# Kernel tuning notes

Measured on AMD Instinct MI355X. Metric: run time of the kernel, lower is better.

The kernel has to match this reference:

```python
import jax, jax.numpy as jnp
import numpy as np

S, N, F_IN, F_OUT = 8, 4096, 128, 128


def setup_inputs() -> dict:
    key = jax.random.key(0)
    ks = jax.random.split(key, 7)
    return {
        "theta": jax.random.normal(ks[0], (S,), dtype=jnp.float32),
        "T_slices": jax.random.normal(ks[1], (S, N, N), dtype=jnp.float32),
        "x": jax.random.normal(ks[2], (N, F_IN), dtype=jnp.float32),
        "a": jax.random.uniform(ks[3], (N, N), dtype=jnp.float32),
        "W_fc": jax.random.normal(ks[4], (F_OUT, F_IN), dtype=jnp.float32) * (1.0 / np.sqrt(F_IN)),
        "b_fc": jax.random.normal(ks[5], (F_OUT,), dtype=jnp.float32) * 0.01,
        "prelu_alpha": jnp.full((F_IN,), 0.25, dtype=jnp.float32),
    }


def reference(theta, T_slices, x, a, W_fc, b_fc, prelu_alpha):
    # q = sum_s theta[s] * T_slices[s]  -> [N, N]
    q = jnp.einsum("s,snm->nm", theta, T_slices)
    # mask by adjacency (the torch code then converts to sparse; math is identical)
    q = q * a
    # diffused features: [N, N] @ [N, F_in] -> [N, F_in]
    out = q @ x
    # per-channel PReLU over the feature dim (num_parameters = input_dim)
    out = jnp.where(out >= 0, out, prelu_alpha * out)
    # final linear: out @ W_fc.T + b_fc -> [N, F_out]
    return out @ W_fc.T + b_fc
```

## Files before the change

### kernel.cpp

```cpp
#include <hip/hip_runtime.h>
#include <stdint.h>

constexpr int N  = 4096;
constexpr int F  = 128;
constexpr int S  = 8;
constexpr int BM = 16;
constexpr int KSPLIT = 8;
constexpr int KRANGE = N / KSPLIT;
constexpr int BK = 32;
constexpr int NCH = KRANGE / BK;
constexpr int NT = 256;

typedef float f4  __attribute__((ext_vector_type(4)));
typedef float f2  __attribute__((ext_vector_type(2)));
typedef short bf16x8 __attribute__((ext_vector_type(8)));
typedef unsigned short us4 __attribute__((ext_vector_type(4)));

__device__ __forceinline__ unsigned short f2bf(float f) {
  union { float f; unsigned int u; } v; v.f = f;
  unsigned int u = v.u + 0x7FFFu + ((v.u >> 16) & 1u);
  return (unsigned short)(u >> 16);
}

__device__ __forceinline__ void bar_sync() {
  asm volatile("s_waitcnt lgkmcnt(0)" ::: "memory");
  __builtin_amdgcn_s_barrier();
  asm volatile("" ::: "memory");
}

__device__ __forceinline__ void vm_drain() {
  asm volatile("s_waitcnt vmcnt(0)" ::: "memory");
}

__device__ __forceinline__ void vm_wait7() {
  asm volatile("s_waitcnt vmcnt(7)" ::: "memory");
}

__device__ __forceinline__ void gload_lds16(const void* g, void* l) {
  __builtin_amdgcn_global_load_lds(
      (const __attribute__((address_space(1))) void*)g,
      (__attribute__((address_space(3))) void*)l, 16, 0, 0);
}

__global__ __launch_bounds__(256, 2) void ggd_xt(
    const float* __restrict__ x, unsigned short* __restrict__ xT) {
  __shared__ float xl[64][132];
  const int t  = threadIdx.x;
  const int k0 = blockIdx.x * 64;

  {
    const int kr = t >> 2, fs = (t & 3) * 32;
    const float* src = x + (size_t)(k0 + kr) * F + fs;
#pragma unroll
    for (int i = 0; i < 8; ++i)
      *(f4*)&xl[kr][fs + i * 4] = *(const f4*)(src + i * 4);
  }
  __syncthreads();
  {
    const int f = t >> 1, kh = (t & 1) * 32;
    us4 o[8];
#pragma unroll
    for (int i = 0; i < 32; ++i)
      o[i >> 2][i & 3] = f2bf(xl[kh + i][f]);
    unsigned short* dst = xT + (size_t)f * N + k0 + kh;
#pragma unroll
    for (int j = 0; j < 8; ++j)
      *(us4*)(dst + j * 4) = o[j];
  }
}

template <bool USE_WS>
__global__ __launch_bounds__(NT, 2) void ggd_diffuse(
    const float* __restrict__ theta,
    const float* __restrict__ Ts,
    const unsigned short* __restrict__ xT,
    const float* __restrict__ a,
    float* __restrict__ dst)
{
  __shared__ float rawT[2][S][BM][BK];
  __shared__ unsigned short xt_lds[3][F][BK];
  __shared__ unsigned short q_lds[2][BM][BK];

  const int t  = threadIdx.x;
  const int rb = blockIdx.x >> 3;
  const int ks = blockIdx.x & 7;
  const int n0 = rb * BM;
  const int k0 = ks * KRANGE;

  float th[S];
#pragma unroll
  for (int s = 0; s < S; ++s) th[s] = theta[s];

  const int wave = t >> 6, lane = t & 63;
  const size_t slice = (size_t)N * N;

  const int qr = t >> 4;
  const int qk = (t & 15) * 2;

  f4 acc[2];
#pragma unroll
  for (int i = 0; i < 2; ++i) acc[i] = (f4)(0.f);

  auto stage_rawT = [&](int c, int buf) {
    const size_t cb = (size_t)(k0 + c * BK) + (lane & 7) * 4;
    const int grow = lane >> 3;
#pragma unroll
    for (int j = 0; j < 4; ++j) {
      const int i = wave * 4 + j;
      const int s = i >> 1;
      const int row = (i & 1) * 8 + grow;
      const float* src = Ts + (size_t)s * slice + (size_t)(n0 + row) * N + cb;
      gload_lds16(src, &rawT[buf][0][0][0] + i * 256);
    }
  };

  auto stage_x = [&](int c, int buf) {
    const uint8_t* xb = (const uint8_t*)xT;
    const size_t kbyte = (size_t)(k0 + c * BK) * 2;
#pragma unroll
    for (int j = 0; j < 2; ++j) {
      const int i = wave * 2 + j;
      const int fr = i * 16 + (lane >> 2);
      const uint8_t* src = xb + (size_t)fr * (N * 2) + kbyte + (lane & 3) * 16;
      gload_lds16(src, &xt_lds[buf][i * 16][0]);
    }
  };

  auto load_a = [&](int c) -> f2 {
    return *(const f2*)(a + (size_t)(n0 + qr) * N + (k0 + c * BK + qk));
  };

  auto qgen = [&](int c1, f2 av) {
    const float* rt = &rawT[c1 & 1][0][qr][qk];
    f2 sum;
    {
      f2 tv = *(const f2*)(rt);
      sum[0] = th[0] * tv[0];
      sum[1] = th[0] * tv[1];
    }
#pragma unroll
    for (int s = 1; s < S; ++s) {
      f2 tv = *(const f2*)(rt + (size_t)s * (BM * BK));
      sum[0] = fmaf(th[s], tv[0], sum[0]);
      sum[1] = fmaf(th[s], tv[1], sum[1]);
    }
    const unsigned int packed =
        (unsigned int)f2bf(av[0] * sum[0]) |
        ((unsigned int)f2bf(av[1] * sum[1]) << 16);
    *(unsigned int*)&q_lds[c1 & 1][qr][qk] = packed;
  };

  auto compute = [&](int c) {
    const unsigned short* qb = &q_lds[c & 1][0][0];
    bf16x8 af = *(const bf16x8*)(qb + (lane & 15) * BK + (lane >> 4) * 8);
    const unsigned short* xb = &xt_lds[c % 3][0][0];
#pragma unroll
    for (int i = 0; i < 2; ++i) {
      const int ft = wave * 2 + i;
      bf16x8 bf = *(const bf16x8*)(xb + (size_t)(ft * 16 + (lane & 15)) * BK +
                                   (lane >> 4) * 8);
      acc[i] = __builtin_amdgcn_mfma_f32_16x16x32_bf16(af, bf, acc[i], 0, 0, 0);
    }
  };

  f2 avE, avO;
  stage_rawT(0, 0);
  stage_x(0, 0);
  avE = load_a(0);
  stage_rawT(1, 1);
  stage_x(1, 1);
  avO = load_a(1);
  vm_drain();
  bar_sync();
  qgen(0, avE);
  bar_sync();

  auto body = [&](int c, f2& av_iss, f2 av_use) {
    const bool iss = (c + 2 < NCH);
    if (iss) {
      stage_rawT(c + 2, c & 1);
      stage_x(c + 2, (c + 2) % 3);
      av_iss = load_a(c + 2);
    }
    compute(c);
    if (iss) vm_wait7(); else vm_drain();
    bar_sync();
    if (c + 1 < NCH) qgen(c + 1, av_use);
    bar_sync();
  };

  for (int cc = 0; cc < NCH; cc += 2) {
    body(cc,     avE, avO);
    body(cc + 1, avO, avE);
  }

  const int crow = n0 + (lane >> 4) * 4;
  const int ccol = lane & 15;
#pragma unroll
  for (int i = 0; i < 2; ++i) {
    const int fo = (wave * 2 + i) * 16 + ccol;
#pragma unroll
    for (int r = 0; r < 4; ++r) {
      const size_t row = (size_t)(crow + r);
      if (USE_WS) {
        dst[((size_t)ks * N + row) * F + fo] = acc[i][r];
      } else {
        atomicAdd(dst + row * F + fo, acc[i][r]);
      }
    }
  }
}

template <bool USE_WS>
__global__ __launch_bounds__(256, 2) void ggd_fc(
    const float* __restrict__ W,
    const float* __restrict__ bfc,
    const float* __restrict__ alpha,
    const float* __restrict__ src,
    float* __restrict__ out)
{
  __shared__ float p_lds[16 * F];
  const int t  = threadIdx.x;
  const int n0 = blockIdx.x * 16;

  {
    const int lr = t >> 4, c8 = (t & 15) * 8;
    f4 v0, v1;
    if (USE_WS) {
      v0 = (f4)(0.f); v1 = (f4)(0.f);
#pragma unroll
      for (int ks = 0; ks < KSPLIT; ++ks) {
        const float* sp = src + ((size_t)ks * N + n0 + lr) * F + c8;
        v0 += *(const f4*)(sp);
        v1 += *(const f4*)(sp + 4);
      }
    } else {
      const float* ip = src + (size_t)(n0 + lr) * F + c8;
      v0 = *(const f4*)(ip);
      v1 = *(const f4*)(ip + 4);
    }
    f4 a0 = *(const f4*)(alpha + c8);
    f4 a1 = *(const f4*)(alpha + c8 + 4);
#pragma unroll
    for (int j = 0; j < 4; ++j) {
      v0[j] = v0[j] >= 0.f ? v0[j] : a0[j] * v0[j];
      v1[j] = v1[j] >= 0.f ? v1[j] : a1[j] * v1[j];
    }
    *(f4*)&p_lds[lr * F + c8]     = v0;
    *(f4*)&p_lds[lr * F + c8 + 4] = v1;
  }
  __syncthreads();

  const int r2  = t >> 5;
  const int fo0 = (t & 31) * 4;
  f4 accA = *(const f4*)(bfc + fo0);
  f4 accB = accA;
#pragma unroll 4
  for (int fi4 = 0; fi4 < F / 4; ++fi4) {
    f4 pA = *(const f4*)&p_lds[r2 * F + fi4 * 4];
    f4 pB = *(const f4*)&p_lds[(r2 + 8) * F + fi4 * 4];
#pragma unroll
    for (int e = 0; e < 4; ++e) {
      f4 wv = *(const f4*)(W + (size_t)(fo0 + e) * F + fi4 * 4);
      accA[e] = fmaf(pA[0], wv[0], fmaf(pA[1], wv[1],
                fmaf(pA[2], wv[2], fmaf(pA[3], wv[3], accA[e]))));
      accB[e] = fmaf(pB[0], wv[0], fmaf(pB[1], wv[1],
                fmaf(pB[2], wv[2], fmaf(pB[3], wv[3], accB[e]))));
    }
  }
  *(f4*)(out + (size_t)(n0 + r2) * F + fo0)     = accA;
  *(f4*)(out + (size_t)(n0 + r2 + 8) * F + fo0) = accB;
}

extern "C" void kernel_launch(void* const* d_in, const int* in_sizes, int n_in,
                              void* d_out, int out_size, void* d_ws, size_t ws_size,
                              hipStream_t stream) {
  const float* theta = (const float*)d_in[0];
  const float* Ts    = (const float*)d_in[1];
  const float* x     = (const float*)d_in[2];
  const float* a     = (const float*)d_in[3];
  const float* W     = (const float*)d_in[4];
  const float* bfc   = (const float*)d_in[5];
  const float* alpha = (const float*)d_in[6];
  float* out = (float*)d_out;

  const size_t part_bytes = (size_t)KSPLIT * N * F * sizeof(float);
  const size_t xt_bytes   = (size_t)N * F * 2;
  if (ws_size >= part_bytes + xt_bytes && d_ws != nullptr) {
    float* parts = (float*)d_ws;
    unsigned short* xT = (unsigned short*)((char*)d_ws + part_bytes);
    ggd_xt<<<dim3(N / 64), dim3(256), 0, stream>>>(x, xT);
    ggd_diffuse<true><<<dim3((N / BM) * KSPLIT), dim3(NT), 0, stream>>>(
        theta, Ts, xT, a, parts);
    ggd_fc<true><<<dim3(N / 16), dim3(256), 0, stream>>>(
        W, bfc, alpha, parts, out);
  } else {
    unsigned short* xT = (unsigned short*)d_ws;
    hipMemsetAsync(out, 0, (size_t)out_size * sizeof(float), stream);
    ggd_xt<<<dim3(N / 64), dim3(256), 0, stream>>>(x, xT);
    ggd_diffuse<false><<<dim3((N / BM) * KSPLIT), dim3(NT), 0, stream>>>(
        theta, Ts, xT, a, out);
    ggd_fc<false><<<dim3(N / 16), dim3(256), 0, stream>>>(
        W, bfc, alpha, out, out);
  }
}
```

Before: 147.2 us.

## Double K chunk, load x fragments straight to registers, one barrier per step

```diff
diff --git a/kernel.cpp b/kernel.cpp
--- a/kernel.cpp
+++ b/kernel.cpp
@@ -7,12 +7,11 @@
 constexpr int BM = 16;
 constexpr int KSPLIT = 8;
 constexpr int KRANGE = N / KSPLIT;
-constexpr int BK = 32;
+constexpr int BK = 64;
 constexpr int NCH = KRANGE / BK;
 constexpr int NT = 256;
 
 typedef float f4  __attribute__((ext_vector_type(4)));
-typedef float f2  __attribute__((ext_vector_type(2)));
 typedef short bf16x8 __attribute__((ext_vector_type(8)));
 typedef unsigned short us4 __attribute__((ext_vector_type(4)));
 
@@ -31,9 +30,11 @@
 __device__ __forceinline__ void vm_drain() {
   asm volatile("s_waitcnt vmcnt(0)" ::: "memory");
 }
-
-__device__ __forceinline__ void vm_wait7() {
-  asm volatile("s_waitcnt vmcnt(7)" ::: "memory");
+__device__ __forceinline__ void vm_wait13() {
+  asm volatile("s_waitcnt vmcnt(13)" ::: "memory");
+}
+__device__ __forceinline__ void vm_wait4() {
+  asm volatile("s_waitcnt vmcnt(4)" ::: "memory");
 }
 
 __device__ __forceinline__ void gload_lds16(const void* g, void* l) {
@@ -41,6 +42,8 @@
       (const __attribute__((address_space(1))) void*)g,
       (__attribute__((address_space(3))) void*)l, 16, 0, 0);
 }
+
+struct BSet { bf16x8 v[4]; };
 
 __global__ __launch_bounds__(256, 2) void ggd_xt(
     const float* __restrict__ x, unsigned short* __restrict__ xT) {
@@ -78,7 +81,6 @@
     float* __restrict__ dst)
 {
   __shared__ float rawT[2][S][BM][BK];
-  __shared__ unsigned short xt_lds[3][F][BK];
   __shared__ unsigned short q_lds[2][BM][BK];
 
   const int t  = threadIdx.x;
@@ -95,104 +97,120 @@
   const size_t slice = (size_t)N * N;
 
   const int qr = t >> 4;
-  const int qk = (t & 15) * 2;
+  const int qk = (t & 15) * 4;
 
   f4 acc[2];
 #pragma unroll
   for (int i = 0; i < 2; ++i) acc[i] = (f4)(0.f);
 
   auto stage_rawT = [&](int c, int buf) {
-    const size_t cb = (size_t)(k0 + c * BK) + (lane & 7) * 4;
-    const int grow = lane >> 3;
-#pragma unroll
-    for (int j = 0; j < 4; ++j) {
-      const int i = wave * 4 + j;
-      const int s = i >> 1;
-      const int row = (i & 1) * 8 + grow;
-      const float* src = Ts + (size_t)s * slice + (size_t)(n0 + row) * N + cb;
+    const int grow = lane >> 4;
+    const size_t cb = (size_t)(k0 + c * BK) + (lane & 15) * 4;
+#pragma unroll
+    for (int j = 0; j < 8; ++j) {
+      const int i = wave * 8 + j;
+      const int s  = i >> 2;
+      const int r4 = (i & 3) * 4;
+      const float* src = Ts + (size_t)s * slice +
+                         (size_t)(n0 + r4 + grow) * N + cb;
       gload_lds16(src, &rawT[buf][0][0][0] + i * 256);
     }
   };
 
-  auto stage_x = [&](int c, int buf) {
-    const uint8_t* xb = (const uint8_t*)xT;
-    const size_t kbyte = (size_t)(k0 + c * BK) * 2;
-#pragma unroll
-    for (int j = 0; j < 2; ++j) {
-      const int i = wave * 2 + j;
-      const int fr = i * 16 + (lane >> 2);
-      const uint8_t* src = xb + (size_t)fr * (N * 2) + kbyte + (lane & 3) * 16;
-      gload_lds16(src, &xt_lds[buf][i * 16][0]);
-    }
-  };
-
-  auto load_a = [&](int c) -> f2 {
-    return *(const f2*)(a + (size_t)(n0 + qr) * N + (k0 + c * BK + qk));
-  };
-
-  auto qgen = [&](int c1, f2 av) {
+  auto bfrag_load = [&](int c, BSet& B) {
+    const int kc = k0 + c * BK;
+#pragma unroll
+    for (int i = 0; i < 2; ++i) {
+      const int fr = (wave * 2 + i) * 16 + (lane & 15);
+#pragma unroll
+      for (int h = 0; h < 2; ++h)
+        B.v[i * 2 + h] = *(const bf16x8*)(xT + (size_t)fr * N + kc + h * 32 +
+                                          (lane >> 4) * 8);
+    }
+  };
+
+  auto load_a = [&](int c) -> f4 {
+    return *(const f4*)(a + (size_t)(n0 + qr) * N + (k0 + c * BK + qk));
+  };
+
+  auto qgen = [&](int c1, f4 av) {
     const float* rt = &rawT[c1 & 1][0][qr][qk];
-    f2 sum;
+    f4 sum;
     {
-      f2 tv = *(const f2*)(rt);
-      sum[0] = th[0] * tv[0];
-      sum[1] = th[0] * tv[1];
+      f4 tv = *(const f4*)rt;
+#pragma unroll
+      for (int j = 0; j < 4; ++j) sum[j] = th[0] * tv[j];
     }
 #pragma unroll
     for (int s = 1; s < S; ++s) {
-      f2 tv = *(const f2*)(rt + (size_t)s * (BM * BK));
-      sum[0] = fmaf(th[s], tv[0], sum[0]);
-      sum[1] = fmaf(th[s], tv[1], sum[1]);
-    }
-    const unsigned int packed =
-        (unsigned int)f2bf(av[0] * sum[0]) |
-        ((unsigned int)f2bf(av[1] * sum[1]) << 16);
-    *(unsigned int*)&q_lds[c1 & 1][qr][qk] = packed;
-  };
-
-  auto compute = [&](int c) {
+      f4 tv = *(const f4*)(rt + (size_t)s * (BM * BK));
+#pragma unroll
+      for (int j = 0; j < 4; ++j) sum[j] = fmaf(th[s], tv[j], sum[j]);
+    }
+    us4 q;
+#pragma unroll
+    for (int j = 0; j < 4; ++j) q[j] = f2bf(av[j] * sum[j]);
+    *(us4*)&q_lds[c1 & 1][qr][qk] = q;
+  };
+
+  auto compute = [&](int c, const BSet& B) {
     const unsigned short* qb = &q_lds[c & 1][0][0];
-    bf16x8 af = *(const bf16x8*)(qb + (lane & 15) * BK + (lane >> 4) * 8);
-    const unsigned short* xb = &xt_lds[c % 3][0][0];
-#pragma unroll
-    for (int i = 0; i < 2; ++i) {
-      const int ft = wave * 2 + i;
-      bf16x8 bf = *(const bf16x8*)(xb + (size_t)(ft * 16 + (lane & 15)) * BK +
+#pragma unroll
+    for (int h = 0; h < 2; ++h) {
+      bf16x8 af = *(const bf16x8*)(qb + (lane & 15) * BK + h * 32 +
                                    (lane >> 4) * 8);
-      acc[i] = __builtin_amdgcn_mfma_f32_16x16x32_bf16(af, bf, acc[i], 0, 0, 0);
-    }
-  };
-
-  f2 avE, avO;
+#pragma unroll
+      for (int i = 0; i < 2; ++i)
+        acc[i] = __builtin_amdgcn_mfma_f32_16x16x32_bf16(af, B.v[i * 2 + h],
+                                                         acc[i], 0, 0, 0);
+    }
+  };
+
+  f4 avE, avO;
+  BSet bE, bO;
+
   stage_rawT(0, 0);
-  stage_x(0, 0);
+  stage_rawT(1, 1);
+  bfrag_load(0, bE);
   avE = load_a(0);
-  stage_rawT(1, 1);
-  stage_x(1, 1);
   avO = load_a(1);
   vm_drain();
   bar_sync();
   qgen(0, avE);
   bar_sync();
 
-  auto body = [&](int c, f2& av_iss, f2 av_use) {
-    const bool iss = (c + 2 < NCH);
-    if (iss) {
+  for (int cc = 0; cc + 1 < NCH - 2; cc += 2) {
+    {
+      const int c = cc;
       stage_rawT(c + 2, c & 1);
-      stage_x(c + 2, (c + 2) % 3);
-      av_iss = load_a(c + 2);
-    }
-    compute(c);
-    if (iss) vm_wait7(); else vm_drain();
+      bfrag_load(c + 1, bO);
+      avE = load_a(c + 2);
+      vm_wait13();
+      compute(c, bE);
+      qgen(c + 1, avO);
+      bar_sync();
+    }
+    {
+      const int c = cc + 1;
+      stage_rawT(c + 2, c & 1);
+      bfrag_load(c + 1, bE);
+      avO = load_a(c + 2);
+      vm_wait13();
+      compute(c, bO);
+      qgen(c + 1, avE);
+      bar_sync();
+    }
+  }
+
+  {
+    const int c = NCH - 2;
+    bfrag_load(c + 1, bO);
+    vm_wait4();
+    compute(c, bE);
+    qgen(c + 1, avO);
     bar_sync();
-    if (c + 1 < NCH) qgen(c + 1, av_use);
-    bar_sync();
-  };
-
-  for (int cc = 0; cc < NCH; cc += 2) {
-    body(cc,     avE, avO);
-    body(cc + 1, avO, avE);
-  }
+  }
+  compute(NCH - 1, bO);
 
   const int crow = n0 + (lane >> 4) * 4;
   const int ccol = lane & 15;
```

Result: faster. 141.3 us (-4.0%).
